# Optimization experiments

Hardware: AMD Instinct MI355X
Metric: run time of the kernel (lower is better)

The kernel has to match this reference:

```python
import jax, jax.numpy as jnp
import numpy as np

SEQ, NV, NH, NR = 32768, 256, 512, 256


def _bern(key, p):
    # torch.bernoulli: sample is non-differentiable
    return (jax.random.uniform(key, p.shape, dtype=p.dtype) < p).astype(p.dtype)


def setup_inputs() -> dict:
    key = jax.random.key(0)
    ks = jax.random.split(key, 8)
    f32 = jnp.float32
    return {
        "v_seq": (jax.random.uniform(ks[0], (SEQ, NV), dtype=f32) < 0.1).astype(f32),
        "W1": jax.random.normal(ks[1], (NV, NH), dtype=f32) * 0.01,
        "bv": jnp.zeros((NV,), f32),
        "bh1": jnp.zeros((NH,), f32),
        "W2": jax.random.normal(ks[2], (NH, NH), dtype=f32) * 0.01,
        "bh2": jnp.zeros((NH,), f32),
        "Wyv": jax.random.normal(ks[3], (NV, NR), dtype=f32) * 1e-4,
        "Wyh1": jax.random.normal(ks[4], (NH, NR), dtype=f32) * 1e-4,
        "Wyh2": jax.random.normal(ks[5], (NH, NR), dtype=f32) * 1e-4,
        "Wvu": jax.random.normal(ks[6], (NV, NR), dtype=f32) * 0.01,
        "Wuu": jax.random.normal(ks[7], (NR, NR), dtype=f32) * 0.01,
        "bu": jnp.zeros((NR,), f32),
        "k": 5,
    }


def reference(v_seq, W1, bv, bh1, W2, bh2, Wyv, Wyh1, Wyh2, Wvu, Wuu, bu, k):
    dtype = v_seq.dtype
    nr = Wuu.shape[0]
    seq_len = v_seq.shape[0]

    # vanilla tanh RNN (abstract _run_rnn in base class)
    def rnn_step(u, v):
        u_new = jnp.tanh(v @ Wvu + u @ Wuu + bu)
        return u_new, u_new

    _, rnn_out = jax.lax.scan(rnn_step, jnp.zeros((nr,), dtype), v_seq)
    shifted = jnp.concatenate([jnp.zeros((1, nr), dtype), rnn_out[:-1]], axis=0)

    bv_t = bv + shifted @ Wyv.T    # [S, NV]
    bh1_t = bh1 + shifted @ Wyh1.T  # [S, NH]
    bh2_t = bh2 + shifted @ Wyh2.T  # [S, NH]

    key = jax.random.key(42)

    # CD-k Gibbs chain, RBM1 (visible <-> hidden1)
    v_sample = v_seq
    mean_v = None
    for _ in range(k):
        key, k1, k2 = jax.random.split(key, 3)
        h = _bern(k1, jax.nn.sigmoid(v_sample @ W1 + bh1_t))
        mean_v = jax.nn.sigmoid(h @ W1.T + bv_t)
        v_sample = _bern(k2, mean_v)

    def free_energy1(v):
        return -(v * bv_t).sum(-1) - jax.nn.softplus(v @ W1 + bh1_t).sum(-1)

    cost1 = (free_energy1(v_seq) - free_energy1(jax.lax.stop_gradient(v_sample))).mean()

    # CD-k Gibbs chain, RBM2 (hidden1 <-> hidden2)
    h1 = jax.nn.sigmoid(v_seq @ W1 + bh1_t)
    h1_sample = h1
    for _ in range(k):
        key, k1, k2 = jax.random.split(key, 3)
        h2 = _bern(k1, jax.nn.sigmoid(h1_sample @ W2 + bh2_t))
        h1_sample = _bern(k2, jax.nn.sigmoid(h2 @ W2.T + bh1_t))

    def free_energy2(h):
        return -(h * bh1_t).sum(-1) - jax.nn.softplus(h @ W2 + bh2_t).sum(-1)

    cost2 = (free_energy2(h1) - free_energy2(jax.lax.stop_gradient(h1_sample))).mean()

    eps = 1e-10
    monitor = (v_seq * jnp.log(mean_v + eps)
               + (1.0 - v_seq) * jnp.log(1.0 - mean_v + eps)).sum() / seq_len
    return (cost1 + cost2, monitor)
```

## Files before the change

kernel.cpp:

```cpp
#include <hip/hip_runtime.h>
#include <cstdint>

#define S_LEN 32768
#define NV 256
#define NH 512
#define NR 256

typedef short bf16x8 __attribute__((ext_vector_type(8)));
typedef float f32x4 __attribute__((ext_vector_type(4)));
typedef unsigned short ushort_t;

__device__ __forceinline__ float b2f(ushort_t u) {
  return __uint_as_float(((uint32_t)u) << 16);
}
__device__ __forceinline__ ushort_t f2b(float f) {
  uint32_t x = __float_as_uint(f);
  uint32_t r = (x + 0x7fffu + ((x >> 16) & 1u)) >> 16;
  return (ushort_t)r;
}

#define GLOAD_LDS16(gsrc, ldst)                                        \
  __builtin_amdgcn_global_load_lds(                                    \
      (const __attribute__((address_space(1))) void*)(gsrc),           \
      (__attribute__((address_space(3))) void*)(ldst), 16, 0, 0)

#define TFR(x0,x1,r) { x0 += x1; x1 = ((x1 << (r)) | (x1 >> (32 - (r)))); x1 ^= x0; }
__host__ __forceinline__ void tf2x32(uint32_t k0, uint32_t k1,
                                     uint32_t x0, uint32_t x1,
                                     uint32_t* o0, uint32_t* o1) {
  uint32_t k2 = k0 ^ k1 ^ 0x1BD11BDAu;
  x0 += k0; x1 += k1;
  TFR(x0,x1,13) TFR(x0,x1,15) TFR(x0,x1,26) TFR(x0,x1,6)
  x0 += k1; x1 += k2 + 1u;
  TFR(x0,x1,17) TFR(x0,x1,29) TFR(x0,x1,16) TFR(x0,x1,24)
  x0 += k2; x1 += k0 + 2u;
  TFR(x0,x1,13) TFR(x0,x1,15) TFR(x0,x1,26) TFR(x0,x1,6)
  x0 += k0; x1 += k1 + 3u;
  TFR(x0,x1,17) TFR(x0,x1,29) TFR(x0,x1,16) TFR(x0,x1,24)
  x0 += k1; x1 += k2 + 4u;
  TFR(x0,x1,13) TFR(x0,x1,15) TFR(x0,x1,26) TFR(x0,x1,6)
  x0 += k2; x1 += k0 + 5u;
  *o0 = x0; *o1 = x1;
}

__device__ __forceinline__ uint32_t fast_hash(uint32_t k0, uint32_t k1, uint32_t idx) {
  uint32_t h = idx ^ k0;
  h *= 0xCC9E2D51u; h = (h << 15) | (h >> 17); h *= 0x1B873593u;
  h ^= k1;
  h ^= h >> 16; h *= 0x85EBCA6Bu;
  h ^= h >> 13; h *= 0xC2B2AE35u;
  h ^= h >> 16;
  return h;
}

__device__ __forceinline__ float wave_reduce(float v) {
#pragma unroll
  for (int o = 32; o > 0; o >>= 1) v += __shfl_down(v, o, 64);
  return v;
}
__device__ __forceinline__ float softplusf(float z) {
  return fmaxf(z, 0.f) + log1pf(expf(-fabsf(z)));
}

#define F_SAMP  4
#define F_H1    8
#define F_FE    16
#define F_MON   32
#define F_DOTB  64
#define F_DOTS  128

struct GemmArgs {
  const ushort_t* A;
  const ushort_t* BT;
  const ushort_t* Ax;
  const ushort_t* BXT;
  const float* bvec;
  int boff;
  ushort_t* C;
  ushort_t* C2;
  const float* vseqf;
  double* fe_acc;
  double* mon_acc;
  float sign;
  uint32_t rk0, rk1;
  int N, K, nbx;
};

template<int FLAGS>
__device__ __forceinline__ void run_gemm(const GemmArgs& g,
                                         const ushort_t* __restrict__ biasm, int ldb,
                                         ushort_t* __restrict__ As0,
                                         ushort_t* __restrict__ As1,
                                         ushort_t* __restrict__ Bs0,
                                         ushort_t* __restrict__ Bs1) {
  const int tid = threadIdx.x;
  const int lane = tid & 63, wave = tid >> 6;
  const int wm = wave >> 1, wn = wave & 1;
  const int q = lane >> 4, l16 = lane & 15;
  const int m0 = blockIdx.y * 128, n0 = blockIdx.x * 128;
  const int N = g.N, K = g.K;
  const int KT = K + 256;

  f32x4 acc[4][4];
#pragma unroll
  for (int mt = 0; mt < 4; mt++)
#pragma unroll
    for (int nt = 0; nt < 4; nt++) acc[mt][nt] = (f32x4){0.f, 0.f, 0.f, 0.f};

  auto stage = [&](ushort_t* As, ushort_t* Bs, int kks) {
    const ushort_t* Ap; const ushort_t* Bp; size_t lda, ldbt; int k0;
    if (kks < K) { Ap = g.A;  Bp = g.BT;  lda = (size_t)K; ldbt = (size_t)K; k0 = kks; }
    else         { Ap = g.Ax; Bp = g.BXT; lda = 256;       ldbt = 256;       k0 = kks - K; }
#pragma unroll
    for (int j = 0; j < 4; j++) {
      int c = j * 256 + tid;
      int r = c >> 3, bl = c & 7, bg = bl ^ (r & 7);
      const int ldso = (j * 256 + wave * 64) * 8;
      GLOAD_LDS16(&Ap[(size_t)(m0 + r) * lda + k0 + bg * 8], &As[ldso]);
      GLOAD_LDS16(&Bp[(size_t)(n0 + r) * ldbt + k0 + bg * 8], &Bs[ldso]);
    }
  };
  auto compute = [&](const ushort_t* As, const ushort_t* Bs) {
#pragma unroll
    for (int c = 0; c < 2; c++) {
      bf16x8 af[4], bf[4];
#pragma unroll
      for (int mt = 0; mt < 4; mt++) {
        int r = wm * 64 + mt * 16 + l16;
        af[mt] = *(const bf16x8*)&As[r * 64 + (((c * 4 + q) ^ (r & 7)) * 8)];
      }
#pragma unroll
      for (int nt = 0; nt < 4; nt++) {
        int r = wn * 64 + nt * 16 + l16;
        bf[nt] = *(const bf16x8*)&Bs[r * 64 + (((c * 4 + q) ^ (r & 7)) * 8)];
      }
#pragma unroll
      for (int mt = 0; mt < 4; mt++)
#pragma unroll
        for (int nt = 0; nt < 4; nt++)
          acc[mt][nt] = __builtin_amdgcn_mfma_f32_16x16x32_bf16(
              af[mt], bf[nt], acc[mt][nt], 0, 0, 0);
    }
  };

  stage(As0, Bs0, 0);
  __syncthreads();
  for (int kk = 0; kk < KT; kk += 128) {
    stage(As1, Bs1, kk + 64);
    compute(As0, Bs0);
    __syncthreads();
    if (kk + 128 < KT) stage(As0, Bs0, kk + 128);
    compute(As1, Bs1);
    __syncthreads();
  }

  float fe_sum = 0.f, mon_sum = 0.f;
#pragma unroll
  for (int mt = 0; mt < 4; mt++) {
#pragma unroll
    for (int nt = 0; nt < 4; nt++) {
      const int gn = n0 + wn * 64 + nt * 16 + l16;
      const int gmb = m0 + wm * 64 + mt * 16 + q * 4;
      const float bvv = g.bvec[gn];
      uint32_t h0 = 0, h1 = 0;
      if constexpr (FLAGS & F_SAMP) {
        uint32_t pb = (uint32_t)((gmb >> 1) * N + gn);
        h0 = fast_hash(g.rk0, g.rk1, pb);
        h1 = fast_hash(g.rk0, g.rk1, pb + (uint32_t)N);
      }
#pragma unroll
      for (int rg = 0; rg < 4; rg++) {
        const int gm = gmb + rg;
        const size_t idx = (size_t)gm * N + gn;
        float z = acc[mt][nt][rg] + bvv;
        float be = 0.f;
        if constexpr (FLAGS & (F_DOTB | F_DOTS))
          be = b2f(biasm[(size_t)gm * ldb + g.boff + gn]);
        if constexpr (FLAGS & (F_SAMP | F_H1 | F_MON)) {
          float e = __expf(-z);
          if constexpr (FLAGS & F_SAMP) {
            uint32_t hb = (rg & 2) ? h1 : h0;
            uint32_t ub = (rg & 1) ? (hb >> 16) : (hb & 0xffffu);
            float uu = (float)ub * (1.0f / 65536.0f);
            bool sbit = fmaf(uu, e, uu) < 1.f;
            g.C[idx] = sbit ? (ushort_t)0x3f80 : (ushort_t)0;
            if constexpr (FLAGS & F_DOTS) fe_sum += sbit ? be : 0.f;
          }
          if constexpr (FLAGS & (F_H1 | F_MON)) {
            float pp = __builtin_amdgcn_rcpf(1.f + e);
            if constexpr (FLAGS & F_H1) g.C2[idx] = f2b(pp);
            if constexpr (FLAGS & F_DOTB) fe_sum += pp * be;
            if constexpr (FLAGS & F_MON) {
              float v = g.vseqf[idx];
              mon_sum += (v != 0.f) ? logf(pp + 1e-10f) : logf(1.f - pp + 1e-10f);
            }
          }
        }
        if constexpr (FLAGS & F_FE) fe_sum += softplusf(z);
      }
    }
  }
  if constexpr (FLAGS & (F_FE | F_DOTB | F_DOTS)) {
    float s = wave_reduce(fe_sum);
    if (lane == 0) atomicAdd(g.fe_acc, (double)(-g.sign * s));
  }
  if constexpr (FLAGS & F_MON) {
    float s = wave_reduce(mon_sum);
    if (lane == 0) atomicAdd(g.mon_acc, (double)s);
  }
}

template<int FLAGS>
__global__ __launch_bounds__(256)
void gemm_samp(GemmArgs g, const ushort_t* __restrict__ biasm, int ldb) {
  __shared__ ushort_t As0[128 * 64], As1[128 * 64];
  __shared__ ushort_t Bs0[128 * 64], Bs1[128 * 64];
  if ((int)blockIdx.x >= g.nbx) return;
  run_gemm<FLAGS>(g, biasm, ldb, As0, As1, Bs0, Bs1);
}

template<int F0, int F1>
__global__ __launch_bounds__(256)
void gemm_pair(GemmArgs g0, GemmArgs g1, const ushort_t* __restrict__ biasm, int ldb) {
  __shared__ ushort_t As0[128 * 64], As1[128 * 64];
  __shared__ ushort_t Bs0[128 * 64], Bs1[128 * 64];
  if (blockIdx.z == 0) {
    if ((int)blockIdx.x >= g0.nbx) return;
    run_gemm<F0>(g0, biasm, ldb, As0, As1, Bs0, Bs1);
  } else {
    if ((int)blockIdx.x >= g1.nbx) return;
    run_gemm<F1>(g1, biasm, ldb, As0, As1, Bs0, Bs1);
  }
}

template<bool OUTF32, bool VDOT>
__global__ __launch_bounds__(256)
void gemm_bias(const ushort_t* __restrict__ A, const ushort_t* __restrict__ BT,
               const float* __restrict__ biasv, ushort_t* __restrict__ Cb,
               float* __restrict__ Cf, const float* __restrict__ vdata,
               double* __restrict__ dacc, int M, int N, int K) {
  __shared__ ushort_t As0[128 * 64], As1[128 * 64];
  __shared__ ushort_t Bs0[128 * 64], Bs1[128 * 64];
  const int tid = threadIdx.x;
  const int lane = tid & 63, wave = tid >> 6;
  const int wm = wave >> 1, wn = wave & 1;
  const int q = lane >> 4, l16 = lane & 15;
  const int m0 = blockIdx.y * 128, n0 = blockIdx.x * 128;

  f32x4 acc[4][4];
#pragma unroll
  for (int i = 0; i < 4; i++)
#pragma unroll
    for (int j = 0; j < 4; j++) acc[i][j] = (f32x4){0.f, 0.f, 0.f, 0.f};

  auto stage = [&](ushort_t* As, ushort_t* Bs, int kk) {
#pragma unroll
    for (int j = 0; j < 4; j++) {
      int c = j * 256 + tid;
      int r = c >> 3, bl = c & 7, bg = bl ^ (r & 7);
      const int ldso = (j * 256 + wave * 64) * 8;
      GLOAD_LDS16(&A[(size_t)(m0 + r) * K + kk + bg * 8], &As[ldso]);
      GLOAD_LDS16(&BT[(size_t)(n0 + r) * K + kk + bg * 8], &Bs[ldso]);
    }
  };
  auto compute = [&](const ushort_t* As, const ushort_t* Bs) {
#pragma unroll
    for (int c = 0; c < 2; c++) {
      bf16x8 af[4], bf[4];
#pragma unroll
      for (int mt = 0; mt < 4; mt++) {
        int r = wm * 64 + mt * 16 + l16;
        af[mt] = *(const bf16x8*)&As[r * 64 + (((c * 4 + q) ^ (r & 7)) * 8)];
      }
#pragma unroll
      for (int nt = 0; nt < 4; nt++) {
        int r = wn * 64 + nt * 16 + l16;
        bf[nt] = *(const bf16x8*)&Bs[r * 64 + (((c * 4 + q) ^ (r & 7)) * 8)];
      }
#pragma unroll
      for (int mt = 0; mt < 4; mt++)
#pragma unroll
        for (int nt = 0; nt < 4; nt++)
          acc[mt][nt] = __builtin_amdgcn_mfma_f32_16x16x32_bf16(
              af[mt], bf[nt], acc[mt][nt], 0, 0, 0);
    }
  };

  stage(As0, Bs0, 0);
  __syncthreads();
  for (int kk = 0; kk < K; kk += 128) {
    stage(As1, Bs1, kk + 64);
    compute(As0, Bs0);
    __syncthreads();
    if (kk + 128 < K) stage(As0, Bs0, kk + 128);
    compute(As1, Bs1);
    __syncthreads();
  }

  float dsum = 0.f;
#pragma unroll
  for (int mt = 0; mt < 4; mt++)
#pragma unroll
    for (int nt = 0; nt < 4; nt++) {
      const int gn = n0 + wn * 64 + nt * 16 + l16;
      const int gmb = m0 + wm * 64 + mt * 16 + q * 4;
      const float bvv = biasv[gn];
#pragma unroll
      for (int rg = 0; rg < 4; rg++) {
        const size_t idx = (size_t)(gmb + rg) * N + gn;
        float z = acc[mt][nt][rg] + bvv;
        if constexpr (OUTF32) Cf[idx] = z; else Cb[idx] = f2b(z);
        if constexpr (VDOT)
          if (n0 < 256) dsum += z * vdata[(size_t)(gmb + rg) * 256 + gn];
      }
    }
  if constexpr (VDOT) {
    if (n0 < 256) {
      float s = wave_reduce(dsum);
      if ((tid & 63) == 0) atomicAdd(dacc, (double)(-s));
    }
  }
}

__global__ __launch_bounds__(1024, 1)
void rnn_scan(const float* __restrict__ Apre, const float* __restrict__ Wuu,
              ushort_t* __restrict__ shifted) {
  const int tid = threadIdx.x;
  const int j = tid >> 2;
  const int s = tid & 3;
  const int t_begin = blockIdx.x * 128;
  const int t_end = t_begin + 128;
  const int t0 = (t_begin >= 16) ? (t_begin - 16) : 0;

  float w[64];
#pragma unroll
  for (int i = 0; i < 64; i++) w[i] = Wuu[(size_t)(s * 64 + i) * 256 + j];

  __shared__ float u[2][280];
  __shared__ float asg[32 * 256];
  if (tid < 256) u[0][(tid >> 6) * 68 + (tid & 63)] = 0.f;
  if (blockIdx.x == 0 && s == 0) shifted[j] = 0;
  __syncthreads();

  const int jp = (j >> 6) * 68 + (j & 63);
  int p = 0;
  for (int tb = t0; tb < t_end; tb += 32) {
    int srow = tb + (tid >> 5);
    if (srow >= S_LEN) srow = S_LEN - 1;
    int scol = (tid & 31) * 8;
    float4 a0 = *(const float4*)&Apre[(size_t)srow * 256 + scol];
    float4 a1 = *(const float4*)&Apre[(size_t)srow * 256 + scol + 4];
    *(float4*)&asg[(tid >> 5) * 256 + scol] = a0;
    *(float4*)&asg[(tid >> 5) * 256 + scol + 4] = a1;
    __syncthreads();
#pragma unroll 1
    for (int i = 0; i < 32; i++) {
      const int t = tb + i;
      if (t >= t_end) break;
      float p0 = 0.f, p1 = 0.f, p2 = 0.f, p3 = 0.f;
#pragma unroll
      for (int qq = 0; qq < 64; qq += 4) {
        float4 uv = *(const float4*)&u[p][s * 68 + qq];
        p0 = fmaf(uv.x, w[qq + 0], p0);
        p1 = fmaf(uv.y, w[qq + 1], p1);
        p2 = fmaf(uv.z, w[qq + 2], p2);
        p3 = fmaf(uv.w, w[qq + 3], p3);
      }
      float ps = (p0 + p1) + (p2 + p3);
      ps += __shfl_xor(ps, 1, 64);
      ps += __shfl_xor(ps, 2, 64);
      float z = asg[i * 256 + j] + ps;
      float e = __expf(2.f * z);
      float unew = 1.f - 2.f * __builtin_amdgcn_rcpf(e + 1.f);
      if (s == 0) {
        u[1 - p][jp] = unew;
        if (t >= t_begin && (t + 1) < S_LEN)
          shifted[(size_t)(t + 1) * 256 + j] = f2b(unew);
      }
      __syncthreads();
      p ^= 1;
    }
  }
}

__global__ __launch_bounds__(256)
void prep_all(const float* __restrict__ v_seq, ushort_t* __restrict__ vseq_bf,
              const float* __restrict__ Wyv, const float* __restrict__ Wyh1,
              const float* __restrict__ Wyh2, ushort_t* __restrict__ Wycat,
              const float* __restrict__ W1, ushort_t* __restrict__ BTw1t,
              ushort_t* __restrict__ BTw1,
              const float* __restrict__ W2, ushort_t* __restrict__ BTw2t,
              ushort_t* __restrict__ BTw2,
              const float* __restrict__ Wvu, ushort_t* __restrict__ BTwvu,
              const float* __restrict__ bv, const float* __restrict__ bh1,
              const float* __restrict__ bh2, float* __restrict__ bveccat) {
  int b = blockIdx.x;
  const int tid = threadIdx.x;
  if (b < 32768) { int i = b * 256 + tid; vseq_bf[i] = f2b(v_seq[i]); return; }
  b -= 32768;
  if (b < 256)  { int i = b * 256 + tid; Wycat[i] = f2b(Wyv[i]); return; }
  b -= 256;
  if (b < 512)  { int i = b * 256 + tid; Wycat[65536 + i] = f2b(Wyh1[i]); return; }
  b -= 512;
  if (b < 512)  { int i = b * 256 + tid; Wycat[196608 + i] = f2b(Wyh2[i]); return; }
  b -= 512;
  if (b < 512)  { int i = b * 256 + tid; BTw1t[i] = f2b(W1[i]); return; }
  b -= 512;
  if (b < 1024) { int i = b * 256 + tid; BTw2t[i] = f2b(W2[i]); return; }
  b -= 1024;
  if (b < 256)  { int i = b * 256 + tid; int r = i >> 8, c = i & 255;
                  BTwvu[c * 256 + r] = f2b(Wvu[i]); return; }
  b -= 256;
  if (b < 512)  { int i = b * 256 + tid; int r = i >> 9, c = i & 511;
                  BTw1[(size_t)c * 256 + r] = f2b(W1[i]); return; }
  b -= 512;
  if (b < 1024) { int i = b * 256 + tid; int r = i >> 9, c = i & 511;
                  BTw2[(size_t)c * 512 + r] = f2b(W2[i]); return; }
  b -= 1024;
  { int i = b * 256 + tid;
    if (i < 1280)
      bveccat[i] = (i < 256) ? bv[i] : (i < 768) ? bh1[i - 256] : bh2[i - 768]; }
}

__global__ void finalize_kernel(const double* __restrict__ acc, float* __restrict__ out) {
  out[0] = (float)(acc[0] / (double)S_LEN);
  out[1] = (float)(acc[1] / (double)S_LEN);
}

extern "C" void kernel_launch(void* const* d_in, const int* in_sizes, int n_in,
                              void* d_out, int out_size, void* d_ws, size_t ws_size,
                              hipStream_t stream) {
  (void)in_sizes; (void)n_in; (void)out_size; (void)ws_size;
  const float* v_seq = (const float*)d_in[0];
  const float* W1    = (const float*)d_in[1];
  const float* bv    = (const float*)d_in[2];
  const float* bh1   = (const float*)d_in[3];
  const float* W2    = (const float*)d_in[4];
  const float* bh2   = (const float*)d_in[5];
  const float* Wyv   = (const float*)d_in[6];
  const float* Wyh1  = (const float*)d_in[7];
  const float* Wyh2  = (const float*)d_in[8];
  const float* Wvu   = (const float*)d_in[9];
  const float* Wuu   = (const float*)d_in[10];
  const float* bu    = (const float*)d_in[11];
  float* out = (float*)d_out;

  const size_t SN = (size_t)S_LEN * NV;
  const size_t SH = (size_t)S_LEN * NH;
  const int NB = NV + NH + NH;
  char* base = (char*)d_ws;
  size_t cur = 0;
  auto take = [&](size_t bytes) { size_t o = cur; cur += (bytes + 255) & ~(size_t)255; return o; };
  double*   acc      = (double*)  (base + take(64));
  ushort_t* BTwvu    = (ushort_t*)(base + take(65536 * 2));
  ushort_t* Wycat    = (ushort_t*)(base + take((size_t)NB * NR * 2));
  float*    bveccat  = (float*)   (base + take(NB * 4));
  ushort_t* BTw1     = (ushort_t*)(base + take(131072 * 2));
  ushort_t* BTw1t    = (ushort_t*)(base + take(131072 * 2));
  ushort_t* BTw2     = (ushort_t*)(base + take(262144 * 2));
  ushort_t* BTw2t    = (ushort_t*)(base + take(262144 * 2));
  ushort_t* vseq_bf  = (ushort_t*)(base + take(SN * 2));
  ushort_t* shifted  = (ushort_t*)(base + take(SN * 2));
  ushort_t* bias_cat = (ushort_t*)(base + take((size_t)S_LEN * NB * 2));
  ushort_t* h1buf    = (ushort_t*)(base + take(SH * 2));
  ushort_t* sampA    = (ushort_t*)(base + take(SH * 2));
  ushort_t* sampB    = (ushort_t*)(base + take(SN * 2));
  ushort_t* sampC    = (ushort_t*)(base + take(SH * 2));
  ushort_t* sampD = h1buf;
  float* Arnn = (float*)bias_cat;

  uint32_t ka[20], kb[20];
  uint32_t K0 = 0u, K1 = 42u;
  for (int it = 0; it < 10; it++) {
    uint32_t n0, n1, a0, a1, b0, b1;
    tf2x32(K0, K1, 0u, 0u, &n0, &n1);
    tf2x32(K0, K1, 0u, 1u, &a0, &a1);
    tf2x32(K0, K1, 0u, 2u, &b0, &b1);
    ka[2 * it] = a0; kb[2 * it] = a1;
    ka[2 * it + 1] = b0; kb[2 * it + 1] = b1;
    K0 = n0; K1 = n1;
  }

  hipMemsetAsync(acc, 0, 2 * sizeof(double), stream);

  dim3 blk(256);
  prep_all<<<dim3(37381), blk, 0, stream>>>(
      v_seq, vseq_bf, Wyv, Wyh1, Wyh2, Wycat, W1, BTw1t, BTw1,
      W2, BTw2t, BTw2, Wvu, BTwvu, bv, bh1, bh2, bveccat);

  const int M = S_LEN;
  gemm_bias<true, false><<<dim3(2, M / 128), blk, 0, stream>>>(
      vseq_bf, BTwvu, bu, nullptr, Arnn, nullptr, nullptr, M, NV, NV);
  rnn_scan<<<dim3(S_LEN / 128), dim3(1024), 0, stream>>>(Arnn, Wuu, shifted);
  gemm_bias<false, true><<<dim3(NB / 128, M / 128), blk, 0, stream>>>(
      shifted, Wycat, bveccat, bias_cat, nullptr, v_seq, acc, M, NB, NR);

  const int OFF_BV = 0, OFF_BH1 = NV, OFF_BH2 = NV + NH;
  auto mk = [&](const ushort_t* A, const ushort_t* BT, int boff, ushort_t* C,
                ushort_t* C2, const float* vs, float sign, int key, int N, int K) {
    GemmArgs g;
    g.A = A; g.BT = BT; g.boff = boff;
    g.Ax = shifted;
    g.BXT = Wycat + (size_t)boff * 256;
    g.bvec = bveccat + boff;
    g.C = C; g.C2 = C2; g.vseqf = vs;
    g.fe_acc = acc; g.mon_acc = acc + 1; g.sign = sign;
    g.rk0 = key >= 0 ? ka[key] : 0; g.rk1 = key >= 0 ? kb[key] : 0;
    g.N = N; g.K = K; g.nbx = N / 128;
    return g;
  };

  gemm_samp<F_SAMP | F_H1 | F_FE | F_DOTB>
      <<<dim3(4, M / 128), blk, 0, stream>>>(
      mk(vseq_bf, BTw1, OFF_BH1, sampA, h1buf, nullptr, 1.0f, 0, NH, NV),
      bias_cat, NB);

  dim3 pg(4, M / 128, 2);
  GemmArgs V[5], Hh[4], A2g[5], B2g[5];
  for (int it = 0; it < 5; it++) {
    if (it > 0)
      Hh[it - 1] = mk(sampB, BTw1, OFF_BH1, sampA, nullptr, nullptr, 0.f,
                      2 * it, NH, NV);
    V[it] = mk(sampA, BTw1t, OFF_BV, sampB, nullptr,
               (it == 4) ? v_seq : nullptr, (it == 4) ? -1.0f : 0.f,
               2 * it + 1, NV, NH);
    A2g[it] = mk((it == 0) ? h1buf : sampD,
                 BTw2, OFF_BH2, sampC, nullptr, nullptr,
                 (it == 0) ? 1.0f : 0.f, 10 + 2 * it, NH, NH);
    B2g[it] = mk(sampC, BTw2t, OFF_BH1, sampD, nullptr, nullptr,
                 (it == 4) ? -1.0f : 0.f, 11 + 2 * it, NH, NH);
  }
  GemmArgs FE1 = mk(sampB, BTw1, OFF_BH1, nullptr, nullptr, nullptr, -1.0f,
                    -1, NH, NV);
  GemmArgs FE2 = mk(sampD, BTw2, OFF_BH2, nullptr, nullptr, nullptr, -1.0f,
                    -1, NH, NH);

  gemm_pair<F_SAMP, F_SAMP | F_FE>
      <<<pg, blk, 0, stream>>>(V[0], A2g[0], bias_cat, NB);
  gemm_pair<F_SAMP, F_SAMP>
      <<<pg, blk, 0, stream>>>(Hh[0], B2g[0], bias_cat, NB);
  gemm_pair<F_SAMP, F_SAMP>
      <<<pg, blk, 0, stream>>>(V[1], A2g[1], bias_cat, NB);
  gemm_pair<F_SAMP, F_SAMP>
      <<<pg, blk, 0, stream>>>(Hh[1], B2g[1], bias_cat, NB);
  gemm_pair<F_SAMP, F_SAMP>
      <<<pg, blk, 0, stream>>>(V[2], A2g[2], bias_cat, NB);
  gemm_pair<F_SAMP, F_SAMP>
      <<<pg, blk, 0, stream>>>(Hh[2], B2g[2], bias_cat, NB);
  gemm_pair<F_SAMP, F_SAMP>
      <<<pg, blk, 0, stream>>>(V[3], A2g[3], bias_cat, NB);
  gemm_pair<F_SAMP, F_SAMP>
      <<<pg, blk, 0, stream>>>(Hh[3], B2g[3], bias_cat, NB);
  gemm_pair<F_SAMP | F_MON | F_DOTS, F_SAMP>
      <<<pg, blk, 0, stream>>>(V[4], A2g[4], bias_cat, NB);
  gemm_pair<F_FE, F_SAMP | F_DOTS>
      <<<pg, blk, 0, stream>>>(FE1, B2g[4], bias_cat, NB);

  gemm_samp<F_FE><<<dim3(4, M / 128), blk, 0, stream>>>(FE2, bias_cat, NB);

  finalize_kernel<<<1, 1, 0, stream>>>(acc, out);
}
```

Before: 1.453 ms.

## Fuse Gibbs chain GEMMs into one persistent band kernel per 64 rows

Replaces the 12 separate paired GEMM launches of both CD-k chains with one kernel. Each block owns a 64-row band of the sequence and walks through every Gibbs step for that band, sweeping N in 256-column chunks, so the whole chain needs no inter-kernel synchronisation. Tiles change from 128x128 to 64x256, and per-GEMM atomic reductions become one register accumulation per block. The cost is less parallelism (512 blocks running serially dependent GEMMs), much larger B-tile LDS traffic per row, and two RBM chains no longer overlapping across blocks.

```diff
diff --git a/kernel.cpp b/kernel.cpp
--- a/kernel.cpp
+++ b/kernel.cpp
@@ -5,6 +5,7 @@
 #define NV 256
 #define NH 512
 #define NR 256
+#define NBIAS 1280
 
 typedef short bf16x8 __attribute__((ext_vector_type(8)));
 typedef float f32x4 __attribute__((ext_vector_type(4)));
@@ -69,168 +70,220 @@
 #define F_DOTB  64
 #define F_DOTS  128
 
-struct GemmArgs {
-  const ushort_t* A;
-  const ushort_t* BT;
-  const ushort_t* Ax;
-  const ushort_t* BXT;
-  const float* bvec;
-  int boff;
-  ushort_t* C;
-  ushort_t* C2;
-  const float* vseqf;
-  double* fe_acc;
-  double* mon_acc;
-  float sign;
-  uint32_t rk0, rk1;
-  int N, K, nbx;
+struct ChainArgs {
+  const ushort_t* vseq_bf;
+  const ushort_t* shifted;
+  const ushort_t* BTw1;
+  const ushort_t* BTw1t;
+  const ushort_t* BTw2;
+  const ushort_t* BTw2t;
+  const ushort_t* Wycat;
+  const float* bveccat;
+  const float* v_seq;
+  const ushort_t* bias_cat;
+  ushort_t* sampA;
+  ushort_t* sampB;
+  ushort_t* sampC;
+  ushort_t* h1buf;
+  double* acc;
+  uint32_t ka[20], kb[20];
 };
 
 template<int FLAGS>
-__device__ __forceinline__ void run_gemm(const GemmArgs& g,
-                                         const ushort_t* __restrict__ biasm, int ldb,
-                                         ushort_t* __restrict__ As0,
-                                         ushort_t* __restrict__ As1,
-                                         ushort_t* __restrict__ Bs0,
-                                         ushort_t* __restrict__ Bs1) {
+__device__ __forceinline__ void band_gemm(
+    int band0,
+    const ushort_t* __restrict__ A, const ushort_t* __restrict__ BT,
+    int N, int K,
+    const ushort_t* __restrict__ Ax, const ushort_t* __restrict__ BXT,
+    const float* __restrict__ bvec,
+    ushort_t* __restrict__ C, ushort_t* __restrict__ C2,
+    const ushort_t* __restrict__ biasm, int boff,
+    const float* __restrict__ vseqf,
+    float sign, uint32_t rk0, uint32_t rk1,
+    float& feR, float& monR,
+    ushort_t* As0, ushort_t* As1, ushort_t* Bs0, ushort_t* Bs1) {
   const int tid = threadIdx.x;
   const int lane = tid & 63, wave = tid >> 6;
-  const int wm = wave >> 1, wn = wave & 1;
   const int q = lane >> 4, l16 = lane & 15;
-  const int m0 = blockIdx.y * 128, n0 = blockIdx.x * 128;
-  const int N = g.N, K = g.K;
   const int KT = K + 256;
-
-  f32x4 acc[4][4];
-#pragma unroll
-  for (int mt = 0; mt < 4; mt++)
-#pragma unroll
-    for (int nt = 0; nt < 4; nt++) acc[mt][nt] = (f32x4){0.f, 0.f, 0.f, 0.f};
-
-  auto stage = [&](ushort_t* As, ushort_t* Bs, int kks) {
-    const ushort_t* Ap; const ushort_t* Bp; size_t lda, ldbt; int k0;
-    if (kks < K) { Ap = g.A;  Bp = g.BT;  lda = (size_t)K; ldbt = (size_t)K; k0 = kks; }
-    else         { Ap = g.Ax; Bp = g.BXT; lda = 256;       ldbt = 256;       k0 = kks - K; }
-#pragma unroll
-    for (int j = 0; j < 4; j++) {
-      int c = j * 256 + tid;
-      int r = c >> 3, bl = c & 7, bg = bl ^ (r & 7);
-      const int ldso = (j * 256 + wave * 64) * 8;
-      GLOAD_LDS16(&Ap[(size_t)(m0 + r) * lda + k0 + bg * 8], &As[ldso]);
-      GLOAD_LDS16(&Bp[(size_t)(n0 + r) * ldbt + k0 + bg * 8], &Bs[ldso]);
-    }
-  };
-  auto compute = [&](const ushort_t* As, const ushort_t* Bs) {
-#pragma unroll
-    for (int c = 0; c < 2; c++) {
-      bf16x8 af[4], bf[4];
-#pragma unroll
-      for (int mt = 0; mt < 4; mt++) {
-        int r = wm * 64 + mt * 16 + l16;
-        af[mt] = *(const bf16x8*)&As[r * 64 + (((c * 4 + q) ^ (r & 7)) * 8)];
-      }
+  const ushort_t* Aband = A + (size_t)band0 * K;
+  const ushort_t* Axband = Ax + (size_t)band0 * 256;
+
+  for (int n0c = 0; n0c < N; n0c += 256) {
+    f32x4 acc[4][4];
+#pragma unroll
+    for (int mt = 0; mt < 4; mt++)
+#pragma unroll
+      for (int nt = 0; nt < 4; nt++) acc[mt][nt] = (f32x4){0.f, 0.f, 0.f, 0.f};
+
+    auto stage = [&](ushort_t* As, ushort_t* Bs, int kks) {
+      const ushort_t* Ap; const ushort_t* Bp; int ld, k0;
+      if (kks < K) { Ap = Aband; Bp = BT + (size_t)n0c * K; ld = K; k0 = kks; }
+      else { Ap = Axband; Bp = BXT + (size_t)n0c * 256; ld = 256; k0 = kks - K; }
+#pragma unroll
+      for (int j = 0; j < 2; j++) {
+        int c = j * 256 + tid;
+        int r = c >> 3, bl = c & 7, bg = bl ^ (r & 7);
+        (void)bl;
+        GLOAD_LDS16(&Ap[(size_t)r * ld + k0 + bg * 8], &As[(j * 256 + wave * 64) * 8]);
+      }
+#pragma unroll
+      for (int j = 0; j < 8; j++) {
+        int c = j * 256 + tid;
+        int r = c >> 3, bl = c & 7, bg = bl ^ (r & 7);
+        (void)bl;
+        GLOAD_LDS16(&Bp[(size_t)r * ld + k0 + bg * 8], &Bs[(j * 256 + wave * 64) * 8]);
+      }
+    };
+    auto compute = [&](const ushort_t* As, const ushort_t* Bs) {
+#pragma unroll
+      for (int c = 0; c < 2; c++) {
+        bf16x8 af[4], bf[4];
+#pragma unroll
+        for (int mt = 0; mt < 4; mt++) {
+          int r = mt * 16 + l16;
+          af[mt] = *(const bf16x8*)&As[r * 64 + (((c * 4 + q) ^ (r & 7)) * 8)];
+        }
+#pragma unroll
+        for (int nt = 0; nt < 4; nt++) {
+          int r = wave * 64 + nt * 16 + l16;
+          bf[nt] = *(const bf16x8*)&Bs[r * 64 + (((c * 4 + q) ^ (r & 7)) * 8)];
+        }
+#pragma unroll
+        for (int mt = 0; mt < 4; mt++)
+#pragma unroll
+          for (int nt = 0; nt < 4; nt++)
+            acc[mt][nt] = __builtin_amdgcn_mfma_f32_16x16x32_bf16(
+                af[mt], bf[nt], acc[mt][nt], 0, 0, 0);
+      }
+    };
+
+    stage(As0, Bs0, 0);
+    __syncthreads();
+    for (int kk = 0; kk < KT; kk += 128) {
+      stage(As1, Bs1, kk + 64);
+      compute(As0, Bs0);
+      __syncthreads();
+      if (kk + 128 < KT) stage(As0, Bs0, kk + 128);
+      compute(As1, Bs1);
+      __syncthreads();
+    }
+
+    float fe_sum = 0.f, mon_sum = 0.f;
+#pragma unroll
+    for (int mt = 0; mt < 4; mt++) {
 #pragma unroll
       for (int nt = 0; nt < 4; nt++) {
-        int r = wn * 64 + nt * 16 + l16;
-        bf[nt] = *(const bf16x8*)&Bs[r * 64 + (((c * 4 + q) ^ (r & 7)) * 8)];
-      }
-#pragma unroll
-      for (int mt = 0; mt < 4; mt++)
-#pragma unroll
-        for (int nt = 0; nt < 4; nt++)
-          acc[mt][nt] = __builtin_amdgcn_mfma_f32_16x16x32_bf16(
-              af[mt], bf[nt], acc[mt][nt], 0, 0, 0);
-    }
-  };
-
-  stage(As0, Bs0, 0);
-  __syncthreads();
-  for (int kk = 0; kk < KT; kk += 128) {
-    stage(As1, Bs1, kk + 64);
-    compute(As0, Bs0);
-    __syncthreads();
-    if (kk + 128 < KT) stage(As0, Bs0, kk + 128);
-    compute(As1, Bs1);
-    __syncthreads();
-  }
-
-  float fe_sum = 0.f, mon_sum = 0.f;
-#pragma unroll
-  for (int mt = 0; mt < 4; mt++) {
-#pragma unroll
-    for (int nt = 0; nt < 4; nt++) {
-      const int gn = n0 + wn * 64 + nt * 16 + l16;
-      const int gmb = m0 + wm * 64 + mt * 16 + q * 4;
-      const float bvv = g.bvec[gn];
-      uint32_t h0 = 0, h1 = 0;
-      if constexpr (FLAGS & F_SAMP) {
-        uint32_t pb = (uint32_t)((gmb >> 1) * N + gn);
-        h0 = fast_hash(g.rk0, g.rk1, pb);
-        h1 = fast_hash(g.rk0, g.rk1, pb + (uint32_t)N);
-      }
-#pragma unroll
-      for (int rg = 0; rg < 4; rg++) {
-        const int gm = gmb + rg;
-        const size_t idx = (size_t)gm * N + gn;
-        float z = acc[mt][nt][rg] + bvv;
-        float be = 0.f;
-        if constexpr (FLAGS & (F_DOTB | F_DOTS))
-          be = b2f(biasm[(size_t)gm * ldb + g.boff + gn]);
-        if constexpr (FLAGS & (F_SAMP | F_H1 | F_MON)) {
-          float e = __expf(-z);
-          if constexpr (FLAGS & F_SAMP) {
-            uint32_t hb = (rg & 2) ? h1 : h0;
-            uint32_t ub = (rg & 1) ? (hb >> 16) : (hb & 0xffffu);
-            float uu = (float)ub * (1.0f / 65536.0f);
-            bool sbit = fmaf(uu, e, uu) < 1.f;
-            g.C[idx] = sbit ? (ushort_t)0x3f80 : (ushort_t)0;
-            if constexpr (FLAGS & F_DOTS) fe_sum += sbit ? be : 0.f;
-          }
-          if constexpr (FLAGS & (F_H1 | F_MON)) {
-            float pp = __builtin_amdgcn_rcpf(1.f + e);
-            if constexpr (FLAGS & F_H1) g.C2[idx] = f2b(pp);
-            if constexpr (FLAGS & F_DOTB) fe_sum += pp * be;
-            if constexpr (FLAGS & F_MON) {
-              float v = g.vseqf[idx];
-              mon_sum += (v != 0.f) ? logf(pp + 1e-10f) : logf(1.f - pp + 1e-10f);
+        const int gn = n0c + wave * 64 + nt * 16 + l16;
+        const int gmb = band0 + mt * 16 + q * 4;
+        const float bvv = bvec[gn];
+        uint32_t h0 = 0, h1 = 0;
+        if constexpr (FLAGS & F_SAMP) {
+          uint32_t pb = (uint32_t)((gmb >> 1) * N + gn);
+          h0 = fast_hash(rk0, rk1, pb);
+          h1 = fast_hash(rk0, rk1, pb + (uint32_t)N);
+        }
+#pragma unroll
+        for (int rg = 0; rg < 4; rg++) {
+          const int gm = gmb + rg;
+          const size_t idx = (size_t)gm * N + gn;
+          float z = acc[mt][nt][rg] + bvv;
+          float be = 0.f;
+          if constexpr (FLAGS & (F_DOTB | F_DOTS))
+            be = b2f(biasm[(size_t)gm * NBIAS + boff + gn]);
+          if constexpr (FLAGS & (F_SAMP | F_H1 | F_MON)) {
+            float e = __expf(-z);
+            if constexpr (FLAGS & F_SAMP) {
+              uint32_t hb = (rg & 2) ? h1 : h0;
+              uint32_t ub = (rg & 1) ? (hb >> 16) : (hb & 0xffffu);
+              float uu = (float)ub * (1.0f / 65536.0f);
+              bool sbit = fmaf(uu, e, uu) < 1.f;
+              C[idx] = sbit ? (ushort_t)0x3f80 : (ushort_t)0;
+              if constexpr (FLAGS & F_DOTS) fe_sum += sbit ? be : 0.f;
+            }
+            if constexpr (FLAGS & (F_H1 | F_MON)) {
+              float pp = __builtin_amdgcn_rcpf(1.f + e);
+              if constexpr (FLAGS & F_H1) C2[idx] = f2b(pp);
+              if constexpr (FLAGS & F_DOTB) fe_sum += pp * be;
+              if constexpr (FLAGS & F_MON) {
+                float v = vseqf[idx];
+                mon_sum += (v != 0.f) ? logf(pp + 1e-10f) : logf(1.f - pp + 1e-10f);
+              }
             }
           }
+          if constexpr (FLAGS & F_FE) fe_sum += softplusf(z);
         }
-        if constexpr (FLAGS & F_FE) fe_sum += softplusf(z);
-      }
-    }
-  }
-  if constexpr (FLAGS & (F_FE | F_DOTB | F_DOTS)) {
-    float s = wave_reduce(fe_sum);
-    if (lane == 0) atomicAdd(g.fe_acc, (double)(-g.sign * s));
-  }
-  if constexpr (FLAGS & F_MON) {
-    float s = wave_reduce(mon_sum);
-    if (lane == 0) atomicAdd(g.mon_acc, (double)s);
-  }
-}
-
-template<int FLAGS>
-__global__ __launch_bounds__(256)
-void gemm_samp(GemmArgs g, const ushort_t* __restrict__ biasm, int ldb) {
-  __shared__ ushort_t As0[128 * 64], As1[128 * 64];
-  __shared__ ushort_t Bs0[128 * 64], Bs1[128 * 64];
-  if ((int)blockIdx.x >= g.nbx) return;
-  run_gemm<FLAGS>(g, biasm, ldb, As0, As1, Bs0, Bs1);
-}
-
-template<int F0, int F1>
-__global__ __launch_bounds__(256)
-void gemm_pair(GemmArgs g0, GemmArgs g1, const ushort_t* __restrict__ biasm, int ldb) {
-  __shared__ ushort_t As0[128 * 64], As1[128 * 64];
-  __shared__ ushort_t Bs0[128 * 64], Bs1[128 * 64];
-  if (blockIdx.z == 0) {
-    if ((int)blockIdx.x >= g0.nbx) return;
-    run_gemm<F0>(g0, biasm, ldb, As0, As1, Bs0, Bs1);
-  } else {
-    if ((int)blockIdx.x >= g1.nbx) return;
-    run_gemm<F1>(g1, biasm, ldb, As0, As1, Bs0, Bs1);
-  }
+      }
+    }
+    feR -= sign * fe_sum;
+    monR += mon_sum;
+    __syncthreads();
+  }
+}
+
+__global__ __launch_bounds__(256, 2)
+void fused_chain(ChainArgs a) {
+  __shared__ ushort_t As0[64 * 64], As1[64 * 64];
+  __shared__ ushort_t Bs0[256 * 64], Bs1[256 * 64];
+  const int band0 = (int)blockIdx.x * 64;
+  float feR = 0.f, monR = 0.f;
+  ushort_t* sampD = a.h1buf;
+  const ushort_t* Wy_v  = a.Wycat;
+  const ushort_t* Wy_h1 = a.Wycat + 256 * 256;
+  const ushort_t* Wy_h2 = a.Wycat + 768 * 256;
+  const float* bv_v  = a.bveccat;
+  const float* bv_h1 = a.bveccat + 256;
+  const float* bv_h2 = a.bveccat + 768;
+
+  band_gemm<F_SAMP | F_H1 | F_FE | F_DOTB>(band0, a.vseq_bf, a.BTw1, 512, 256,
+      a.shifted, Wy_h1, bv_h1, a.sampA, a.h1buf, a.bias_cat, 256, nullptr,
+      1.0f, a.ka[0], a.kb[0], feR, monR, As0, As1, Bs0, Bs1);
+
+#pragma unroll 1
+  for (int it = 0; it < 4; it++) {
+    band_gemm<F_SAMP>(band0, a.sampA, a.BTw1t, 256, 512, a.shifted, Wy_v, bv_v,
+        a.sampB, nullptr, a.bias_cat, 0, nullptr, 0.f,
+        a.ka[2 * it + 1], a.kb[2 * it + 1], feR, monR, As0, As1, Bs0, Bs1);
+    band_gemm<F_SAMP>(band0, a.sampB, a.BTw1, 512, 256, a.shifted, Wy_h1, bv_h1,
+        a.sampA, nullptr, a.bias_cat, 256, nullptr, 0.f,
+        a.ka[2 * it + 2], a.kb[2 * it + 2], feR, monR, As0, As1, Bs0, Bs1);
+  }
+  band_gemm<F_SAMP | F_MON | F_DOTS>(band0, a.sampA, a.BTw1t, 256, 512,
+      a.shifted, Wy_v, bv_v, a.sampB, nullptr, a.bias_cat, 0, a.v_seq,
+      -1.0f, a.ka[9], a.kb[9], feR, monR, As0, As1, Bs0, Bs1);
+  band_gemm<F_FE>(band0, a.sampB, a.BTw1, 512, 256, a.shifted, Wy_h1, bv_h1,
+      nullptr, nullptr, a.bias_cat, 256, nullptr, -1.0f, 0u, 0u,
+      feR, monR, As0, As1, Bs0, Bs1);
+
+  band_gemm<F_SAMP | F_FE>(band0, a.h1buf, a.BTw2, 512, 512, a.shifted, Wy_h2,
+      bv_h2, a.sampC, nullptr, a.bias_cat, 768, nullptr, 1.0f,
+      a.ka[10], a.kb[10], feR, monR, As0, As1, Bs0, Bs1);
+  band_gemm<F_SAMP>(band0, a.sampC, a.BTw2t, 512, 512, a.shifted, Wy_h1, bv_h1,
+      sampD, nullptr, a.bias_cat, 256, nullptr, 0.f,
+      a.ka[11], a.kb[11], feR, monR, As0, As1, Bs0, Bs1);
+#pragma unroll 1
+  for (int it = 1; it < 4; it++) {
+    band_gemm<F_SAMP>(band0, sampD, a.BTw2, 512, 512, a.shifted, Wy_h2, bv_h2,
+        a.sampC, nullptr, a.bias_cat, 768, nullptr, 0.f,
+        a.ka[10 + 2 * it], a.kb[10 + 2 * it], feR, monR, As0, As1, Bs0, Bs1);
+    band_gemm<F_SAMP>(band0, a.sampC, a.BTw2t, 512, 512, a.shifted, Wy_h1, bv_h1,
+        sampD, nullptr, a.bias_cat, 256, nullptr, 0.f,
+        a.ka[11 + 2 * it], a.kb[11 + 2 * it], feR, monR, As0, As1, Bs0, Bs1);
+  }
+  band_gemm<F_SAMP>(band0, sampD, a.BTw2, 512, 512, a.shifted, Wy_h2, bv_h2,
+      a.sampC, nullptr, a.bias_cat, 768, nullptr, 0.f,
+      a.ka[18], a.kb[18], feR, monR, As0, As1, Bs0, Bs1);
+  band_gemm<F_SAMP | F_DOTS>(band0, a.sampC, a.BTw2t, 512, 512, a.shifted,
+      Wy_h1, bv_h1, sampD, nullptr, a.bias_cat, 256, nullptr, -1.0f,
+      a.ka[19], a.kb[19], feR, monR, As0, As1, Bs0, Bs1);
+  band_gemm<F_FE>(band0, sampD, a.BTw2, 512, 512, a.shifted, Wy_h2, bv_h2,
+      nullptr, nullptr, a.bias_cat, 768, nullptr, -1.0f, 0u, 0u,
+      feR, monR, As0, As1, Bs0, Bs1);
+
+  float s = wave_reduce(feR);
+  if ((threadIdx.x & 63) == 0) atomicAdd(a.acc, (double)s);
+  s = wave_reduce(monR);
+  if ((threadIdx.x & 63) == 0) atomicAdd(a.acc + 1, (double)s);
 }
 
 template<bool OUTF32, bool VDOT>
@@ -258,6 +311,7 @@
     for (int j = 0; j < 4; j++) {
       int c = j * 256 + tid;
       int r = c >> 3, bl = c & 7, bg = bl ^ (r & 7);
+      (void)bl;
       const int ldso = (j * 256 + wave * 64) * 8;
       GLOAD_LDS16(&A[(size_t)(m0 + r) * K + kk + bg * 8], &As[ldso]);
       GLOAD_LDS16(&BT[(size_t)(n0 + r) * K + kk + bg * 8], &Bs[ldso]);
@@ -447,26 +501,24 @@
 
   const size_t SN = (size_t)S_LEN * NV;
   const size_t SH = (size_t)S_LEN * NH;
-  const int NB = NV + NH + NH;
   char* base = (char*)d_ws;
   size_t cur = 0;
   auto take = [&](size_t bytes) { size_t o = cur; cur += (bytes + 255) & ~(size_t)255; return o; };
   double*   acc      = (double*)  (base + take(64));
   ushort_t* BTwvu    = (ushort_t*)(base + take(65536 * 2));
-  ushort_t* Wycat    = (ushort_t*)(base + take((size_t)NB * NR * 2));
-  float*    bveccat  = (float*)   (base + take(NB * 4));
+  ushort_t* Wycat    = (ushort_t*)(base + take((size_t)NBIAS * NR * 2));
+  float*    bveccat  = (float*)   (base + take(NBIAS * 4));
   ushort_t* BTw1     = (ushort_t*)(base + take(131072 * 2));
   ushort_t* BTw1t    = (ushort_t*)(base + take(131072 * 2));
   ushort_t* BTw2     = (ushort_t*)(base + take(262144 * 2));
   ushort_t* BTw2t    = (ushort_t*)(base + take(262144 * 2));
   ushort_t* vseq_bf  = (ushort_t*)(base + take(SN * 2));
   ushort_t* shifted  = (ushort_t*)(base + take(SN * 2));
-  ushort_t* bias_cat = (ushort_t*)(base + take((size_t)S_LEN * NB * 2));
+  ushort_t* bias_cat = (ushort_t*)(base + take((size_t)S_LEN * NBIAS * 2));
   ushort_t* h1buf    = (ushort_t*)(base + take(SH * 2));
   ushort_t* sampA    = (ushort_t*)(base + take(SH * 2));
   ushort_t* sampB    = (ushort_t*)(base + take(SN * 2));
   ushort_t* sampC    = (ushort_t*)(base + take(SH * 2));
-  ushort_t* sampD = h1buf;
   float* Arnn = (float*)bias_cat;
 
   uint32_t ka[20], kb[20];
@@ -492,71 +544,18 @@
   gemm_bias<true, false><<<dim3(2, M / 128), blk, 0, stream>>>(
       vseq_bf, BTwvu, bu, nullptr, Arnn, nullptr, nullptr, M, NV, NV);
   rnn_scan<<<dim3(S_LEN / 128), dim3(1024), 0, stream>>>(Arnn, Wuu, shifted);
-  gemm_bias<false, true><<<dim3(NB / 128, M / 128), blk, 0, stream>>>(
-      shifted, Wycat, bveccat, bias_cat, nullptr, v_seq, acc, M, NB, NR);
-
-  const int OFF_BV = 0, OFF_BH1 = NV, OFF_BH2 = NV + NH;
-  auto mk = [&](const ushort_t* A, const ushort_t* BT, int boff, ushort_t* C,
-                ushort_t* C2, const float* vs, float sign, int key, int N, int K) {
-    GemmArgs g;
-    g.A = A; g.BT = BT; g.boff = boff;
-    g.Ax = shifted;
-    g.BXT = Wycat + (size_t)boff * 256;
-    g.bvec = bveccat + boff;
-    g.C = C; g.C2 = C2; g.vseqf = vs;
-    g.fe_acc = acc; g.mon_acc = acc + 1; g.sign = sign;
-    g.rk0 = key >= 0 ? ka[key] : 0; g.rk1 = key >= 0 ? kb[key] : 0;
-    g.N = N; g.K = K; g.nbx = N / 128;
-    return g;
-  };
-
-  gemm_samp<F_SAMP | F_H1 | F_FE | F_DOTB>
-      <<<dim3(4, M / 128), blk, 0, stream>>>(
-      mk(vseq_bf, BTw1, OFF_BH1, sampA, h1buf, nullptr, 1.0f, 0, NH, NV),
-      bias_cat, NB);
-
-  dim3 pg(4, M / 128, 2);
-  GemmArgs V[5], Hh[4], A2g[5], B2g[5];
-  for (int it = 0; it < 5; it++) {
-    if (it > 0)
-      Hh[it - 1] = mk(sampB, BTw1, OFF_BH1, sampA, nullptr, nullptr, 0.f,
-                      2 * it, NH, NV);
-    V[it] = mk(sampA, BTw1t, OFF_BV, sampB, nullptr,
-               (it == 4) ? v_seq : nullptr, (it == 4) ? -1.0f : 0.f,
-               2 * it + 1, NV, NH);
-    A2g[it] = mk((it == 0) ? h1buf : sampD,
-                 BTw2, OFF_BH2, sampC, nullptr, nullptr,
-                 (it == 0) ? 1.0f : 0.f, 10 + 2 * it, NH, NH);
-    B2g[it] = mk(sampC, BTw2t, OFF_BH1, sampD, nullptr, nullptr,
-                 (it == 4) ? -1.0f : 0.f, 11 + 2 * it, NH, NH);
-  }
-  GemmArgs FE1 = mk(sampB, BTw1, OFF_BH1, nullptr, nullptr, nullptr, -1.0f,
-                    -1, NH, NV);
-  GemmArgs FE2 = mk(sampD, BTw2, OFF_BH2, nullptr, nullptr, nullptr, -1.0f,
-                    -1, NH, NH);
-
-  gemm_pair<F_SAMP, F_SAMP | F_FE>
-      <<<pg, blk, 0, stream>>>(V[0], A2g[0], bias_cat, NB);
-  gemm_pair<F_SAMP, F_SAMP>
-      <<<pg, blk, 0, stream>>>(Hh[0], B2g[0], bias_cat, NB);
-  gemm_pair<F_SAMP, F_SAMP>
-      <<<pg, blk, 0, stream>>>(V[1], A2g[1], bias_cat, NB);
-  gemm_pair<F_SAMP, F_SAMP>
-      <<<pg, blk, 0, stream>>>(Hh[1], B2g[1], bias_cat, NB);
-  gemm_pair<F_SAMP, F_SAMP>
-      <<<pg, blk, 0, stream>>>(V[2], A2g[2], bias_cat, NB);
-  gemm_pair<F_SAMP, F_SAMP>
-      <<<pg, blk, 0, stream>>>(Hh[2], B2g[2], bias_cat, NB);
-  gemm_pair<F_SAMP, F_SAMP>
-      <<<pg, blk, 0, stream>>>(V[3], A2g[3], bias_cat, NB);
-  gemm_pair<F_SAMP, F_SAMP>
-      <<<pg, blk, 0, stream>>>(Hh[3], B2g[3], bias_cat, NB);
-  gemm_pair<F_SAMP | F_MON | F_DOTS, F_SAMP>
-      <<<pg, blk, 0, stream>>>(V[4], A2g[4], bias_cat, NB);
-  gemm_pair<F_FE, F_SAMP | F_DOTS>
-      <<<pg, blk, 0, stream>>>(FE1, B2g[4], bias_cat, NB);
-
-  gemm_samp<F_FE><<<dim3(4, M / 128), blk, 0, stream>>>(FE2, bias_cat, NB);
+  gemm_bias<false, true><<<dim3(NBIAS / 128, M / 128), blk, 0, stream>>>(
+      shifted, Wycat, bveccat, bias_cat, nullptr, v_seq, acc, M, NBIAS, NR);
+
+  ChainArgs a;
+  a.vseq_bf = vseq_bf; a.shifted = shifted;
+  a.BTw1 = BTw1; a.BTw1t = BTw1t; a.BTw2 = BTw2; a.BTw2t = BTw2t;
+  a.Wycat = Wycat; a.bveccat = bveccat; a.v_seq = v_seq; a.bias_cat = bias_cat;
+  a.sampA = sampA; a.sampB = sampB; a.sampC = sampC; a.h1buf = h1buf;
+  a.acc = acc;
+  for (int i = 0; i < 20; i++) { a.ka[i] = ka[i]; a.kb[i] = kb[i]; }
+
+  fused_chain<<<dim3(S_LEN / 64), blk, 0, stream>>>(a);
 
   finalize_kernel<<<1, 1, 0, stream>>>(acc, out);
 }
```

Measured after the change: 1.753 ms. 1.21x slower.
